# Kernel optimization log

Hardware: AMD Instinct MI355X
Metric: run time of the kernel (lower is better)

Reference implementation:

```python
import jax, jax.numpy as jnp
import numpy as np

D_MODEL = 64
D_K = 64
D_V = 64
N_HEADS = 4
D_FF = 64
D_HALF = 32  # d_model / 2 in the sca_* MLPs


def _layer_norm(x, eps=1e-5):
    m = jnp.mean(x, axis=-1, keepdims=True)
    v = jnp.var(x, axis=-1, keepdims=True)
    return (x - m) / jnp.sqrt(v + eps)


def _sca(u, w1, w2):
    # nn.Sequential(Linear(64,32), ReLU, Linear(32,1)), no bias
    return jax.nn.relu(u @ w1) @ w2  # [B,1,1]


def setup_inputs() -> dict:
    key = jax.random.key(0)
    ks = jax.random.split(key, 20)
    B, L = 128, 512

    def lin(k, fan_in, fan_out):
        bound = 1.0 / np.sqrt(fan_in)
        return jax.random.uniform(k, (fan_in, fan_out), jnp.float32, -bound, bound)

    inp = {
        "input": jax.random.normal(ks[0], (B, L, D_MODEL), jnp.float32),
        "attn_mask": jax.random.bernoulli(ks[1], 0.1, (B, L, L)),
        "input_u": jax.random.normal(ks[2], (B, 1, D_MODEL), jnp.float32),
        "W_Q": lin(ks[3], D_MODEL, N_HEADS * D_K),
        "W_K": lin(ks[4], D_MODEL, N_HEADS * D_K),
        "W_V": lin(ks[5], D_MODEL, N_HEADS * D_V),
        "U_Q": lin(ks[6], D_MODEL, D_K),
        "U_K": lin(ks[7], D_MODEL, D_K),
        "U_V": lin(ks[8], D_MODEL, D_V),
        "sq1": lin(ks[9], D_MODEL, D_HALF),
        "sq2": lin(ks[10], D_HALF, 1),
        "sk1": lin(ks[11], D_MODEL, D_HALF),
        "sk2": lin(ks[12], D_HALF, 1),
        "sv1": lin(ks[13], D_MODEL, D_HALF),
        "sv2": lin(ks[14], D_HALF, 1),
        "fc": lin(ks[15], N_HEADS * D_V, D_MODEL),
        "ff1": lin(ks[16], D_MODEL, D_FF),
        "ff2": lin(ks[17], D_FF, D_MODEL),
    }
    return inp


def reference(input, attn_mask, input_u, W_Q, W_K, W_V, U_Q, U_K, U_V,
              sq1, sq2, sk1, sk2, sv1, sv2, fc, ff1, ff2):
    B, L, _ = input.shape
    scale = 1.0 / np.sqrt(D_K).astype(np.float32)

    # multi-head projections: [B, H, L, d]
    Q = (input @ W_Q).reshape(B, L, N_HEADS, D_K).transpose(0, 2, 1, 3)
    K = (input @ W_K).reshape(B, L, N_HEADS, D_K).transpose(0, 2, 1, 3)
    V = (input @ W_V).reshape(B, L, N_HEADS, D_V).transpose(0, 2, 1, 3)

    # per-batch scalar gates from input_u: [B,1,1]
    s_q = _sca(input_u, sq1, sq2)
    s_k = _sca(input_u, sk1, sk2)
    s_v = _sca(input_u, sv1, sv2)

    # single-head u projections, gated; broadcast over heads later
    u_Q = (input @ U_Q) * s_q  # [B, L, d_k]
    u_K = (input @ U_K) * s_k  # [B, L, d_k]
    u_V = (input @ U_V) * s_v  # [B, L, d_v]

    scores = jnp.einsum('bhqd,bhkd->bhqk', Q, K) * scale
    scores = scores + (jnp.einsum('bqd,bkd->bqk', u_Q, u_K) * scale)[:, None]
    scores = jnp.where(attn_mask[:, None], jnp.float32(-1e9), scores)
    attn = jax.nn.softmax(scores, axis=-1)  # [B, H, L, L]

    context = jnp.einsum('bhqk,bhkd->bhqd', attn, V + u_V[:, None])
    context = context.transpose(0, 2, 1, 3).reshape(B, L, N_HEADS * D_V)

    out = context @ fc  # dropout is identity in eval
    enc = _layer_norm(out + input)

    # position-wise FFN with residual + layernorm
    ffn = jax.nn.relu(enc @ ff1) @ ff2
    enc_outputs = _layer_norm(ffn + enc)
    return (enc_outputs, attn)
```

## Files before the change

### kernel.cpp

```cpp
#include <hip/hip_runtime.h>

typedef unsigned char  u8;
typedef unsigned short u16;
typedef unsigned int   u32;

typedef __attribute__((ext_vector_type(8))) short bf16x8;
typedef __attribute__((ext_vector_type(4))) float f32x4;

__device__ __forceinline__ u16 f2bf(float f) {
  union { float f; u32 u; } v; v.f = f;
  u32 u = v.u;
  u32 r = u + 0x7fffu + ((u >> 16) & 1u);
  return (u16)(r >> 16);
}
__device__ __forceinline__ float bf2f(u16 h) {
  union { u32 u; float f; } v; v.u = ((u32)h) << 16;
  return v.f;
}
__device__ __forceinline__ bf16x8 pack8(float4 a, float4 b) {
  bf16x8 r;
  r[0] = (short)f2bf(a.x); r[1] = (short)f2bf(a.y);
  r[2] = (short)f2bf(a.z); r[3] = (short)f2bf(a.w);
  r[4] = (short)f2bf(b.x); r[5] = (short)f2bf(b.y);
  r[6] = (short)f2bf(b.z); r[7] = (short)f2bf(b.w);
  return r;
}
__device__ __forceinline__ f32x4 mfma16(bf16x8 a, bf16x8 b, f32x4 c) {
  return __builtin_amdgcn_mfma_f32_16x16x32_bf16(a, b, c, 0, 0, 0);
}

__global__ void kflaginit(u32* flags) { flags[0] = 0; flags[1] = 0; }

__global__ void kscan(const u32* __restrict__ m, u32* __restrict__ flags) {
  int gid = blockIdx.x * 256 + threadIdx.x;
  const uint4* p = (const uint4*)m;
  u32 gt = 0, fp = 0;
#pragma unroll
  for (int i = 0; i < 4; ++i) {
    uint4 v = p[gid * 4 + i];
    gt |= (u32)((v.x > 1u) | (v.y > 1u) | (v.z > 1u) | (v.w > 1u));
    fp |= (u32)((v.x == 0x3F800000u) | (v.y == 0x3F800000u) |
                (v.z == 0x3F800000u) | (v.w == 0x3F800000u));
  }
  if (gt) flags[0] = 1;
  if (fp) flags[1] = 1;
}

__global__ void kconv(const void* __restrict__ m, const u32* __restrict__ flags,
                      u8* __restrict__ out) {
  int gid = blockIdx.x * 256 + threadIdx.x;
  u32 isf = flags[1], isb = flags[0];
  uchar4 o;
  if (isf) {
    float4 v = ((const float4*)m)[gid];
    o.x = v.x != 0.f; o.y = v.y != 0.f; o.z = v.z != 0.f; o.w = v.w != 0.f;
  } else if (isb) {
    uchar4 v = ((const uchar4*)m)[gid];
    o.x = v.x != 0; o.y = v.y != 0; o.z = v.z != 0; o.w = v.w != 0;
  } else {
    uint4 v = ((const uint4*)m)[gid];
    o.x = v.x != 0; o.y = v.y != 0; o.z = v.z != 0; o.w = v.w != 0;
  }
  ((uchar4*)out)[gid] = o;
}

__global__ void kgates(const float* __restrict__ iu,
                       const float* __restrict__ q1, const float* __restrict__ q2,
                       const float* __restrict__ k1, const float* __restrict__ k2,
                       const float* __restrict__ v1, const float* __restrict__ v2,
                       float* __restrict__ gates) {
  int b = blockIdx.x, t = threadIdx.x;
  __shared__ float u[64];
  u[t] = iu[b * 64 + t];
  __syncthreads();
  const float* w1[3] = {q1, k1, v1};
  const float* w2[3] = {q2, k2, v2};
#pragma unroll
  for (int m = 0; m < 3; ++m) {
    float p = 0.f;
    if (t < 32) {
      float h = 0.f;
      for (int i = 0; i < 64; ++i) h += u[i] * w1[m][i * 32 + t];
      h = fmaxf(h, 0.f);
      p = h * w2[m][t];
    }
    for (int off = 32; off >= 1; off >>= 1) p += __shfl_xor(p, off);
    if (t == 0) gates[m * 128 + b] = p;
  }
}

__launch_bounds__(256, 1)
__global__ void kproj_qk(const float* __restrict__ x,
                         const float* __restrict__ wq, const float* __restrict__ uq,
                         const float* __restrict__ wk, const float* __restrict__ uk,
                         const float* __restrict__ gates,
                         u16* __restrict__ qc, u16* __restrict__ qu,
                         u16* __restrict__ kc, u16* __restrict__ ku) {
  __shared__ u16 XT[64 * 136];
  __shared__ u16 WT[640 * 72];
  int b = blockIdx.x >> 3, l0 = (blockIdx.x & 7) * 64, t = threadIdx.x;
  {
    int tok = t >> 2, i0 = (t & 3) * 16;
    const float4* s = (const float4*)(x + ((size_t)(b * 512 + l0 + tok)) * 64 + i0);
    *(bf16x8*)&XT[tok * 136 + i0]     = pack8(s[0], s[1]);
    *(bf16x8*)&XT[tok * 136 + i0 + 8] = pack8(s[2], s[3]);
  }
  for (int i = 0; i < 64; ++i) { int e = t + i * 256; WT[(e & 255) * 72 + (e >> 8)] = (short)f2bf(wq[e]); }
  for (int i = 0; i < 16; ++i) { int e = t + i * 256; WT[(256 + (e & 63)) * 72 + (e >> 6)] = (short)f2bf(uq[e]); }
  for (int i = 0; i < 64; ++i) { int e = t + i * 256; WT[(320 + (e & 255)) * 72 + (e >> 8)] = (short)f2bf(wk[e]); }
  for (int i = 0; i < 16; ++i) { int e = t + i * 256; WT[(576 + (e & 63)) * 72 + (e >> 6)] = (short)f2bf(uk[e]); }
  __syncthreads();

  int w = t >> 6, lane = t & 63, lrow = lane & 15, lgrp = lane >> 4;
  bf16x8 af[4][2];
#pragma unroll
  for (int m = 0; m < 4; ++m)
#pragma unroll
    for (int fs = 0; fs < 2; ++fs)
      af[m][fs] = *(const bf16x8*)&XT[(m * 16 + lrow) * 136 + fs * 32 + lgrp * 8];

  float sq = gates[b], sk = gates[128 + b];
  const f32x4 fz = {0.f, 0.f, 0.f, 0.f};
#pragma unroll
  for (int part = 0; part < 2; ++part) {
    f32x4 acc[4][5];
#pragma unroll
    for (int m = 0; m < 4; ++m)
#pragma unroll
      for (int nt = 0; nt < 5; ++nt) acc[m][nt] = fz;
#pragma unroll
    for (int fs = 0; fs < 2; ++fs)
#pragma unroll
      for (int nt = 0; nt < 5; ++nt) {
        bf16x8 bf = *(const bf16x8*)&WT[(part * 320 + w * 80 + nt * 16 + lrow) * 72 + fs * 32 + lgrp * 8];
#pragma unroll
        for (int m = 0; m < 4; ++m)
          acc[m][nt] = mfma16(af[m][fs], bf, acc[m][nt]);
      }
    u16* dstC = part ? kc : qc;
    u16* dstU = part ? ku : qu;
    float presc = part ? 1.0f : 0.125f;
    float g = (part ? sk : sq) * presc;
#pragma unroll
    for (int nt = 0; nt < 5; ++nt) {
      int ncol = w * 80 + nt * 16 + lrow;
#pragma unroll
      for (int m = 0; m < 4; ++m)
#pragma unroll
        for (int j = 0; j < 4; ++j) {
          int l = l0 + m * 16 + lgrp * 4 + j;
          float v = acc[m][nt][j];
          if (ncol < 256) {
            dstC[(((size_t)(b * 4 + (ncol >> 6)) * 512) + l) * 64 + (ncol & 63)] = (short)f2bf(v * presc);
          } else {
            dstU[((size_t)b * 512 + l) * 64 + (ncol - 256)] = (short)f2bf(v * g);
          }
        }
    }
  }
}

__launch_bounds__(256, 1)
__global__ void kproj_v(const float* __restrict__ x,
                        const float* __restrict__ wv, const float* __restrict__ uv,
                        const float* __restrict__ gates, u16* __restrict__ vpt) {
  __shared__ u16 XT[64 * 136];
  __shared__ u16 WT[320 * 72];
  __shared__ float Vs[64 * 328];
  int b = blockIdx.x >> 3, l0 = (blockIdx.x & 7) * 64, t = threadIdx.x;
  {
    int tok = t >> 2, i0 = (t & 3) * 16;
    const float4* s = (const float4*)(x + ((size_t)(b * 512 + l0 + tok)) * 64 + i0);
    *(bf16x8*)&XT[tok * 136 + i0]     = pack8(s[0], s[1]);
    *(bf16x8*)&XT[tok * 136 + i0 + 8] = pack8(s[2], s[3]);
  }
  for (int i = 0; i < 64; ++i) { int e = t + i * 256; WT[(e & 255) * 72 + (e >> 8)] = (short)f2bf(wv[e]); }
  for (int i = 0; i < 16; ++i) { int e = t + i * 256; WT[(256 + (e & 63)) * 72 + (e >> 6)] = (short)f2bf(uv[e]); }
  __syncthreads();

  int w = t >> 6, lane = t & 63, lrow = lane & 15, lgrp = lane >> 4;
  bf16x8 af[4][2];
#pragma unroll
  for (int m = 0; m < 4; ++m)
#pragma unroll
    for (int fs = 0; fs < 2; ++fs)
      af[m][fs] = *(const bf16x8*)&XT[(m * 16 + lrow) * 136 + fs * 32 + lgrp * 8];

  const f32x4 fz = {0.f, 0.f, 0.f, 0.f};
  f32x4 acc[4][5];
#pragma unroll
  for (int m = 0; m < 4; ++m)
#pragma unroll
    for (int nt = 0; nt < 5; ++nt) acc[m][nt] = fz;
#pragma unroll
  for (int fs = 0; fs < 2; ++fs)
#pragma unroll
    for (int nt = 0; nt < 5; ++nt) {
      bf16x8 bf = *(const bf16x8*)&WT[(w * 80 + nt * 16 + lrow) * 72 + fs * 32 + lgrp * 8];
#pragma unroll
      for (int m = 0; m < 4; ++m)
        acc[m][nt] = mfma16(af[m][fs], bf, acc[m][nt]);
    }
#pragma unroll
  for (int nt = 0; nt < 5; ++nt)
#pragma unroll
    for (int m = 0; m < 4; ++m)
#pragma unroll
      for (int j = 0; j < 4; ++j)
        Vs[(m * 16 + lgrp * 4 + j) * 328 + w * 80 + nt * 16 + lrow] = acc[m][nt][j];
  __syncthreads();

  float sv = gates[256 + b];
#pragma unroll
  for (int p = 0; p < 4; ++p) {
    int hd = p * 64 + (t >> 2);
    int d = hd & 63;
    int tok0 = (t & 3) * 16;
    bf16x8 v0, v1;
#pragma unroll
    for (int i = 0; i < 8; ++i) {
      int tok = tok0 + i;
      v0[i] = (short)f2bf(Vs[tok * 328 + hd] + Vs[tok * 328 + 256 + d] * sv);
    }
#pragma unroll
    for (int i = 0; i < 8; ++i) {
      int tok = tok0 + 8 + i;
      v1[i] = (short)f2bf(Vs[tok * 328 + hd] + Vs[tok * 328 + 256 + d] * sv);
    }
    size_t base = (((size_t)(b * 4 + (hd >> 6)) * 64) + d) * 512 + l0 + tok0;
    *(bf16x8*)&vpt[base] = v0;
    *(bf16x8*)&vpt[base + 8] = v1;
  }
}

__launch_bounds__(256, 1)
__global__ void kattn(const u16* __restrict__ qc, const u16* __restrict__ qu,
                      const u16* __restrict__ kc, const u16* __restrict__ ku,
                      const u16* __restrict__ vpt, const u8* __restrict__ maskb,
                      float* __restrict__ aout, u16* __restrict__ ctx) {
  __shared__ char smem[133120];
  u16* QT = (u16*)smem;
  u16* KT = (u16*)(smem + 17408);
  u16* Pl = (u16*)smem;
  u16* Vt = (u16*)(smem + 66560);

  int bid = blockIdx.x;
  int bh = bid >> 3, qt = bid & 7;
  int b = bh >> 2, hh = bh & 3;
  int q0 = qt * 64;
  int t = threadIdx.x, w = t >> 6, lane = t & 63, lrow = lane & 15, lgrp = lane >> 4;

  {
    int tok = t >> 2, c0 = (t & 3) * 32;
    const u16* src = (c0 < 64)
      ? qc + ((size_t)bh * 512 + q0 + tok) * 64 + c0
      : qu + ((size_t)b  * 512 + q0 + tok) * 64 + (c0 - 64);
#pragma unroll
    for (int i = 0; i < 4; ++i)
      *(bf16x8*)&QT[tok * 136 + c0 + i * 8] = *(const bf16x8*)&src[i * 8];
  }
  {
    int d = t >> 2, c0 = (t & 3) * 128;
    const u16* src = vpt + ((size_t)bh * 64 + d) * 512 + c0;
#pragma unroll
    for (int i = 0; i < 16; ++i)
      *(bf16x8*)&Vt[d * 520 + c0 + i * 8] = *(const bf16x8*)&src[i * 8];
  }

  const f32x4 fz = {0.f, 0.f, 0.f, 0.f};
  f32x4 sacc[32];
#pragma unroll
  for (int i = 0; i < 32; ++i) sacc[i] = fz;

#pragma unroll
  for (int kt = 0; kt < 4; ++kt) {
    __syncthreads();
    {
      int r = t >> 1, c0 = (t & 1) * 64;
      const u16* src = (c0 == 0)
        ? kc + ((size_t)bh * 512 + kt * 128 + r) * 64
        : ku + ((size_t)b  * 512 + kt * 128 + r) * 64;
#pragma unroll
      for (int i = 0; i < 8; ++i)
        *(bf16x8*)&KT[r * 136 + c0 + i * 8] = *(const bf16x8*)&src[i * 8];
    }
    __syncthreads();
#pragma unroll
    for (int fs = 0; fs < 4; ++fs) {
      bf16x8 a = *(const bf16x8*)&QT[(w * 16 + lrow) * 136 + fs * 32 + lgrp * 8];
#pragma unroll
      for (int nt = 0; nt < 8; ++nt) {
        bf16x8 bf = *(const bf16x8*)&KT[(nt * 16 + lrow) * 136 + fs * 32 + lgrp * 8];
        sacc[kt * 8 + nt] = mfma16(a, bf, sacc[kt * 8 + nt]);
      }
    }
  }
  __syncthreads();

  int qloc0 = w * 16 + lgrp * 4;
  const u8* mrow = maskb + ((size_t)b * 512 + q0 + qloc0) * 512;
  float mj[4] = {-3.0e38f, -3.0e38f, -3.0e38f, -3.0e38f};
#pragma unroll
  for (int i = 0; i < 32; ++i) {
    int kpos = (i >> 3) * 128 + (i & 7) * 16 + lrow;
#pragma unroll
    for (int j = 0; j < 4; ++j) {
      float s = sacc[i][j];
      if (mrow[(size_t)j * 512 + kpos]) s = -1.0e9f;
      sacc[i][j] = s;
      mj[j] = fmaxf(mj[j], s);
    }
  }
#pragma unroll
  for (int j = 0; j < 4; ++j) {
    mj[j] = fmaxf(mj[j], __shfl_xor(mj[j], 1));
    mj[j] = fmaxf(mj[j], __shfl_xor(mj[j], 2));
    mj[j] = fmaxf(mj[j], __shfl_xor(mj[j], 4));
    mj[j] = fmaxf(mj[j], __shfl_xor(mj[j], 8));
  }
  float lj[4] = {0.f, 0.f, 0.f, 0.f};
#pragma unroll
  for (int i = 0; i < 32; ++i)
#pragma unroll
    for (int j = 0; j < 4; ++j) {
      float p = __expf(sacc[i][j] - mj[j]);
      sacc[i][j] = p;
      lj[j] += p;
    }
#pragma unroll
  for (int j = 0; j < 4; ++j) {
    lj[j] += __shfl_xor(lj[j], 1);
    lj[j] += __shfl_xor(lj[j], 2);
    lj[j] += __shfl_xor(lj[j], 4);
    lj[j] += __shfl_xor(lj[j], 8);
  }
  float inv[4];
#pragma unroll
  for (int j = 0; j < 4; ++j) inv[j] = 1.0f / lj[j];

  size_t ab = ((size_t)bh * 512 + q0 + qloc0) * 512;
#pragma unroll
  for (int i = 0; i < 32; ++i) {
    int kpos = (i >> 3) * 128 + (i & 7) * 16 + lrow;
#pragma unroll
    for (int j = 0; j < 4; ++j) {
      float aval = sacc[i][j] * inv[j];
      aout[ab + (size_t)j * 512 + kpos] = aval;
      Pl[(qloc0 + j) * 520 + kpos] = (short)f2bf(aval);
    }
  }

  f32x4 cacc[4];
#pragma unroll
  for (int nt = 0; nt < 4; ++nt) cacc[nt] = fz;
#pragma unroll
  for (int ks = 0; ks < 16; ++ks) {
    bf16x8 a = *(const bf16x8*)&Pl[(w * 16 + lrow) * 520 + ks * 32 + lgrp * 8];
#pragma unroll
    for (int nt = 0; nt < 4; ++nt) {
      bf16x8 bf = *(const bf16x8*)&Vt[(nt * 16 + lrow) * 520 + ks * 32 + lgrp * 8];
      cacc[nt] = mfma16(a, bf, cacc[nt]);
    }
  }
#pragma unroll
  for (int nt = 0; nt < 4; ++nt)
#pragma unroll
    for (int j = 0; j < 4; ++j) {
      int q = q0 + qloc0 + j;
      ctx[((size_t)b * 512 + q) * 256 + hh * 64 + nt * 16 + lrow] = (short)f2bf(cacc[nt][j]);
    }
}

__launch_bounds__(256, 1)
__global__ void kffn(const u16* __restrict__ ctx, const float* __restrict__ x,
                     const float* __restrict__ fcw, const float* __restrict__ f1w,
                     const float* __restrict__ f2w, float* __restrict__ out) {
  __shared__ u16 CT[64 * 264];
  __shared__ u16 FCT[64 * 264];
  __shared__ u16 F1T[64 * 72];
  __shared__ u16 F2T[64 * 72];
  __shared__ float ENC[64 * 68];
  __shared__ u16 EBF[64 * 72];
  __shared__ u16 HBF[64 * 72];
  int b = blockIdx.x >> 3, l0 = (blockIdx.x & 7) * 64, t = threadIdx.x;
  {
    int tok = t >> 2, c0 = (t & 3) * 64;
    const u16* src = ctx + ((size_t)(b * 512 + l0 + tok)) * 256 + c0;
#pragma unroll
    for (int i = 0; i < 8; ++i)
      *(bf16x8*)&CT[tok * 264 + c0 + i * 8] = *(const bf16x8*)&src[i * 8];
  }
  for (int i = 0; i < 64; ++i) { int e = t + i * 256; FCT[(e & 63) * 264 + (e >> 6)] = (short)f2bf(fcw[e]); }
  for (int i = 0; i < 16; ++i) { int e = t + i * 256; F1T[(e & 63) * 72 + (e >> 6)] = (short)f2bf(f1w[e]); }
  for (int i = 0; i < 16; ++i) { int e = t + i * 256; F2T[(e & 63) * 72 + (e >> 6)] = (short)f2bf(f2w[e]); }
  __syncthreads();

  int w = t >> 6, lane = t & 63, lrow = lane & 15, lgrp = lane >> 4;
  int row = w * 16 + lgrp * 4;
  const f32x4 fz = {0.f, 0.f, 0.f, 0.f};

  f32x4 acc[4];
#pragma unroll
  for (int nt = 0; nt < 4; ++nt) acc[nt] = fz;
#pragma unroll
  for (int ks = 0; ks < 8; ++ks) {
    bf16x8 a = *(const bf16x8*)&CT[(w * 16 + lrow) * 264 + ks * 32 + lgrp * 8];
#pragma unroll
    for (int nt = 0; nt < 4; ++nt)
      acc[nt] = mfma16(a, *(const bf16x8*)&FCT[(nt * 16 + lrow) * 264 + ks * 32 + lgrp * 8], acc[nt]);
  }
  const float* xb = x + ((size_t)(b * 512 + l0)) * 64;
#pragma unroll
  for (int nt = 0; nt < 4; ++nt)
#pragma unroll
    for (int j = 0; j < 4; ++j)
      acc[nt][j] += xb[(row + j) * 64 + nt * 16 + lrow];

  float mean[4], rstd[4];
#pragma unroll
  for (int j = 0; j < 4; ++j) {
    float s = acc[0][j] + acc[1][j] + acc[2][j] + acc[3][j];
    s += __shfl_xor(s, 1); s += __shfl_xor(s, 2); s += __shfl_xor(s, 4); s += __shfl_xor(s, 8);
    mean[j] = s * 0.015625f;
  }
#pragma unroll
  for (int j = 0; j < 4; ++j) {
    float d0 = acc[0][j] - mean[j], d1 = acc[1][j] - mean[j];
    float d2 = acc[2][j] - mean[j], d3 = acc[3][j] - mean[j];
    float s = d0 * d0 + d1 * d1 + d2 * d2 + d3 * d3;
    s += __shfl_xor(s, 1); s += __shfl_xor(s, 2); s += __shfl_xor(s, 4); s += __shfl_xor(s, 8);
    rstd[j] = 1.0f / sqrtf(s * 0.015625f + 1e-5f);
  }
#pragma unroll
  for (int nt = 0; nt < 4; ++nt)
#pragma unroll
    for (int j = 0; j < 4; ++j) {
      float v = (acc[nt][j] - mean[j]) * rstd[j];
      ENC[(row + j) * 68 + nt * 16 + lrow] = v;
      EBF[(row + j) * 72 + nt * 16 + lrow] = (short)f2bf(v);
    }

  f32x4 h4[4];
#pragma unroll
  for (int nt = 0; nt < 4; ++nt) h4[nt] = fz;
#pragma unroll
  for (int ks = 0; ks < 2; ++ks) {
    bf16x8 a = *(const bf16x8*)&EBF[(w * 16 + lrow) * 72 + ks * 32 + lgrp * 8];
#pragma unroll
    for (int nt = 0; nt < 4; ++nt)
      h4[nt] = mfma16(a, *(const bf16x8*)&F1T[(nt * 16 + lrow) * 72 + ks * 32 + lgrp * 8], h4[nt]);
  }
#pragma unroll
  for (int nt = 0; nt < 4; ++nt)
#pragma unroll
    for (int j = 0; j < 4; ++j)
      HBF[(row + j) * 72 + nt * 16 + lrow] = (short)f2bf(fmaxf(h4[nt][j], 0.f));

  f32x4 o4[4];
#pragma unroll
  for (int nt = 0; nt < 4; ++nt) o4[nt] = fz;
#pragma unroll
  for (int ks = 0; ks < 2; ++ks) {
    bf16x8 a = *(const bf16x8*)&HBF[(w * 16 + lrow) * 72 + ks * 32 + lgrp * 8];
#pragma unroll
    for (int nt = 0; nt < 4; ++nt)
      o4[nt] = mfma16(a, *(const bf16x8*)&F2T[(nt * 16 + lrow) * 72 + ks * 32 + lgrp * 8], o4[nt]);
  }
#pragma unroll
  for (int nt = 0; nt < 4; ++nt)
#pragma unroll
    for (int j = 0; j < 4; ++j)
      o4[nt][j] += ENC[(row + j) * 68 + nt * 16 + lrow];

  float mean2[4], rstd2[4];
#pragma unroll
  for (int j = 0; j < 4; ++j) {
    float s = o4[0][j] + o4[1][j] + o4[2][j] + o4[3][j];
    s += __shfl_xor(s, 1); s += __shfl_xor(s, 2); s += __shfl_xor(s, 4); s += __shfl_xor(s, 8);
    mean2[j] = s * 0.015625f;
  }
#pragma unroll
  for (int j = 0; j < 4; ++j) {
    float d0 = o4[0][j] - mean2[j], d1 = o4[1][j] - mean2[j];
    float d2 = o4[2][j] - mean2[j], d3 = o4[3][j] - mean2[j];
    float s = d0 * d0 + d1 * d1 + d2 * d2 + d3 * d3;
    s += __shfl_xor(s, 1); s += __shfl_xor(s, 2); s += __shfl_xor(s, 4); s += __shfl_xor(s, 8);
    rstd2[j] = 1.0f / sqrtf(s * 0.015625f + 1e-5f);
  }
#pragma unroll
  for (int nt = 0; nt < 4; ++nt)
#pragma unroll
    for (int j = 0; j < 4; ++j)
      out[((size_t)(b * 512 + l0) + row + j) * 64 + nt * 16 + lrow] =
          (o4[nt][j] - mean2[j]) * rstd2[j];
}

extern "C" void kernel_launch(void* const* d_in, const int* in_sizes, int n_in,
                              void* d_out, int out_size, void* d_ws, size_t ws_size,
                              hipStream_t stream) {
  const float* x   = (const float*)d_in[0];
  const void*  msk = d_in[1];
  const float* iu  = (const float*)d_in[2];
  const float* wq  = (const float*)d_in[3];
  const float* wk  = (const float*)d_in[4];
  const float* wv  = (const float*)d_in[5];
  const float* uq  = (const float*)d_in[6];
  const float* uk  = (const float*)d_in[7];
  const float* uv  = (const float*)d_in[8];
  const float* q1  = (const float*)d_in[9];
  const float* q2  = (const float*)d_in[10];
  const float* k1  = (const float*)d_in[11];
  const float* k2  = (const float*)d_in[12];
  const float* v1  = (const float*)d_in[13];
  const float* v2  = (const float*)d_in[14];
  const float* fcw = (const float*)d_in[15];
  const float* f1w = (const float*)d_in[16];
  const float* f2w = (const float*)d_in[17];
  float* out = (float*)d_out;

  char* ws = (char*)d_ws;
  u32*   flags = (u32*)ws;
  float* gates = (float*)(ws + 64);
  u16* qc  = (u16*)(ws + 4096);
  u16* qu  = (u16*)(ws + 33558528);
  u16* kc  = (u16*)(ws + 41947136);
  u16* ku  = (u16*)(ws + 75501568);
  u16* vpt = (u16*)(ws + 83890176);
  u8*  mb  = (u8*) (ws + 117444608);
  u16* ctx = (u16*)(ws + 150999040);

  kflaginit<<<dim3(1), dim3(1), 0, stream>>>(flags);
  kscan<<<dim3(1024), dim3(256), 0, stream>>>((const u32*)msk, flags);
  kconv<<<dim3(32768), dim3(256), 0, stream>>>(msk, flags, mb);
  kgates<<<dim3(128), dim3(64), 0, stream>>>(iu, q1, q2, k1, k2, v1, v2, gates);
  kproj_qk<<<dim3(1024), dim3(256), 0, stream>>>(x, wq, uq, wk, uk, gates, qc, qu, kc, ku);
  kproj_v<<<dim3(1024), dim3(256), 0, stream>>>(x, wv, uv, gates, vpt);
  kattn<<<dim3(4096), dim3(256), 0, stream>>>(qc, qu, kc, ku, vpt, mb, out + 4194304, ctx);
  kffn<<<dim3(1024), dim3(256), 0, stream>>>(ctx, x, fcw, f1w, f2w, out);
}
```

Baseline: 538.1 us.

## Split attention key range across two wave groups and shrink LDS for occupancy

The attention kernel now runs 512 threads, with two wave groups each handling half the keys for the same 64 queries. Row max and row sum are combined through shared memory, and V plus the probability tile are streamed in 128-key chunks instead of being held whole. This cuts LDS from about 130KB to 52KB and halves the per-thread accumulator registers, so more blocks can be resident per CU. Blocks are also remapped so consecutive block IDs touch different batches and heads, which changes how mask and K reuse falls across the machine. The cost is extra barriers and cross-wave reductions.

```diff
diff --git a/kernel.cpp b/kernel.cpp
--- a/kernel.cpp
+++ b/kernel.cpp
@@ -233,81 +233,79 @@
   }
 }
 
-__launch_bounds__(256, 1)
+__launch_bounds__(512, 4)
 __global__ void kattn(const u16* __restrict__ qc, const u16* __restrict__ qu,
                       const u16* __restrict__ kc, const u16* __restrict__ ku,
                       const u16* __restrict__ vpt, const u8* __restrict__ maskb,
                       float* __restrict__ aout, u16* __restrict__ ctx) {
-  __shared__ char smem[133120];
+  __shared__ char smem[53248];
   u16* QT = (u16*)smem;
   u16* KT = (u16*)(smem + 17408);
-  u16* Pl = (u16*)smem;
-  u16* Vt = (u16*)(smem + 66560);
+  float* SMm = (float*)(smem + 52224);
+  float* SMl = (float*)(smem + 52736);
+  u16* Vt = (u16*)smem;
+  u16* Pl = (u16*)(smem + 17408);
 
   int bid = blockIdx.x;
-  int bh = bid >> 3, qt = bid & 7;
-  int b = bh >> 2, hh = bh & 3;
+  int logical = (bid & 7) * 512 + (bid >> 3);
+  int b = logical >> 5;
+  int r5 = logical & 31;
+  int qt = r5 >> 2, hh = r5 & 3;
+  int bh = b * 4 + hh;
   int q0 = qt * 64;
+
   int t = threadIdx.x, w = t >> 6, lane = t & 63, lrow = lane & 15, lgrp = lane >> 4;
+  int qsub = w & 3, g = w >> 2, g64 = g * 64;
 
   {
-    int tok = t >> 2, c0 = (t & 3) * 32;
+    int tok = t >> 3, c0 = (t & 7) * 16;
     const u16* src = (c0 < 64)
       ? qc + ((size_t)bh * 512 + q0 + tok) * 64 + c0
       : qu + ((size_t)b  * 512 + q0 + tok) * 64 + (c0 - 64);
-#pragma unroll
-    for (int i = 0; i < 4; ++i)
-      *(bf16x8*)&QT[tok * 136 + c0 + i * 8] = *(const bf16x8*)&src[i * 8];
-  }
-  {
-    int d = t >> 2, c0 = (t & 3) * 128;
-    const u16* src = vpt + ((size_t)bh * 64 + d) * 512 + c0;
-#pragma unroll
-    for (int i = 0; i < 16; ++i)
-      *(bf16x8*)&Vt[d * 520 + c0 + i * 8] = *(const bf16x8*)&src[i * 8];
+    *(bf16x8*)&QT[tok * 136 + c0]     = *(const bf16x8*)&src[0];
+    *(bf16x8*)&QT[tok * 136 + c0 + 8] = *(const bf16x8*)&src[8];
   }
 
   const f32x4 fz = {0.f, 0.f, 0.f, 0.f};
-  f32x4 sacc[32];
-#pragma unroll
-  for (int i = 0; i < 32; ++i) sacc[i] = fz;
+  f32x4 acc[16];
+#pragma unroll
+  for (int i = 0; i < 16; ++i) acc[i] = fz;
 
 #pragma unroll
   for (int kt = 0; kt < 4; ++kt) {
     __syncthreads();
     {
-      int r = t >> 1, c0 = (t & 1) * 64;
-      const u16* src = (c0 == 0)
-        ? kc + ((size_t)bh * 512 + kt * 128 + r) * 64
-        : ku + ((size_t)b  * 512 + kt * 128 + r) * 64;
-#pragma unroll
-      for (int i = 0; i < 8; ++i)
+      int r = t >> 2, c0 = (t & 3) * 32;
+      const u16* src = (c0 < 64)
+        ? kc + ((size_t)bh * 512 + kt * 128 + r) * 64 + c0
+        : ku + ((size_t)b  * 512 + kt * 128 + r) * 64 + (c0 - 64);
+#pragma unroll
+      for (int i = 0; i < 4; ++i)
         *(bf16x8*)&KT[r * 136 + c0 + i * 8] = *(const bf16x8*)&src[i * 8];
     }
     __syncthreads();
 #pragma unroll
     for (int fs = 0; fs < 4; ++fs) {
-      bf16x8 a = *(const bf16x8*)&QT[(w * 16 + lrow) * 136 + fs * 32 + lgrp * 8];
-#pragma unroll
-      for (int nt = 0; nt < 8; ++nt) {
-        bf16x8 bf = *(const bf16x8*)&KT[(nt * 16 + lrow) * 136 + fs * 32 + lgrp * 8];
-        sacc[kt * 8 + nt] = mfma16(a, bf, sacc[kt * 8 + nt]);
+      bf16x8 a = *(const bf16x8*)&QT[(qsub * 16 + lrow) * 136 + fs * 32 + lgrp * 8];
+#pragma unroll
+      for (int nt = 0; nt < 4; ++nt) {
+        bf16x8 bf = *(const bf16x8*)&KT[(g64 + nt * 16 + lrow) * 136 + fs * 32 + lgrp * 8];
+        acc[kt * 4 + nt] = mfma16(a, bf, acc[kt * 4 + nt]);
       }
     }
   }
-  __syncthreads();
-
-  int qloc0 = w * 16 + lgrp * 4;
+
+  int qloc0 = qsub * 16 + lgrp * 4;
   const u8* mrow = maskb + ((size_t)b * 512 + q0 + qloc0) * 512;
   float mj[4] = {-3.0e38f, -3.0e38f, -3.0e38f, -3.0e38f};
 #pragma unroll
-  for (int i = 0; i < 32; ++i) {
-    int kpos = (i >> 3) * 128 + (i & 7) * 16 + lrow;
+  for (int i = 0; i < 16; ++i) {
+    int kpos = (i >> 2) * 128 + g64 + (i & 3) * 16 + lrow;
 #pragma unroll
     for (int j = 0; j < 4; ++j) {
-      float s = sacc[i][j];
+      float s = acc[i][j];
       if (mrow[(size_t)j * 512 + kpos]) s = -1.0e9f;
-      sacc[i][j] = s;
+      acc[i][j] = s;
       mj[j] = fmaxf(mj[j], s);
     }
   }
@@ -318,13 +316,21 @@
     mj[j] = fmaxf(mj[j], __shfl_xor(mj[j], 4));
     mj[j] = fmaxf(mj[j], __shfl_xor(mj[j], 8));
   }
+  if (lrow == 0) {
+#pragma unroll
+    for (int j = 0; j < 4; ++j) SMm[g64 + qloc0 + j] = mj[j];
+  }
+  __syncthreads();
+  float gm[4];
+#pragma unroll
+  for (int j = 0; j < 4; ++j) gm[j] = fmaxf(SMm[qloc0 + j], SMm[64 + qloc0 + j]);
   float lj[4] = {0.f, 0.f, 0.f, 0.f};
 #pragma unroll
-  for (int i = 0; i < 32; ++i)
+  for (int i = 0; i < 16; ++i)
 #pragma unroll
     for (int j = 0; j < 4; ++j) {
-      float p = __expf(sacc[i][j] - mj[j]);
-      sacc[i][j] = p;
+      float p = __expf(acc[i][j] - gm[j]);
+      acc[i][j] = p;
       lj[j] += p;
     }
 #pragma unroll
@@ -334,41 +340,59 @@
     lj[j] += __shfl_xor(lj[j], 4);
     lj[j] += __shfl_xor(lj[j], 8);
   }
+  if (lrow == 0) {
+#pragma unroll
+    for (int j = 0; j < 4; ++j) SMl[g64 + qloc0 + j] = lj[j];
+  }
+  __syncthreads();
   float inv[4];
 #pragma unroll
-  for (int j = 0; j < 4; ++j) inv[j] = 1.0f / lj[j];
+  for (int j = 0; j < 4; ++j) inv[j] = 1.0f / (SMl[qloc0 + j] + SMl[64 + qloc0 + j]);
 
   size_t ab = ((size_t)bh * 512 + q0 + qloc0) * 512;
 #pragma unroll
-  for (int i = 0; i < 32; ++i) {
-    int kpos = (i >> 3) * 128 + (i & 7) * 16 + lrow;
+  for (int i = 0; i < 16; ++i) {
+    int kpos = (i >> 2) * 128 + g64 + (i & 3) * 16 + lrow;
 #pragma unroll
     for (int j = 0; j < 4; ++j) {
-      float aval = sacc[i][j] * inv[j];
-      aout[ab + (size_t)j * 512 + kpos] = aval;
-      Pl[(qloc0 + j) * 520 + kpos] = (short)f2bf(aval);
-    }
-  }
-
-  f32x4 cacc[4];
-#pragma unroll
-  for (int nt = 0; nt < 4; ++nt) cacc[nt] = fz;
-#pragma unroll
-  for (int ks = 0; ks < 16; ++ks) {
-    bf16x8 a = *(const bf16x8*)&Pl[(w * 16 + lrow) * 520 + ks * 32 + lgrp * 8];
-#pragma unroll
-    for (int nt = 0; nt < 4; ++nt) {
-      bf16x8 bf = *(const bf16x8*)&Vt[(nt * 16 + lrow) * 520 + ks * 32 + lgrp * 8];
-      cacc[nt] = mfma16(a, bf, cacc[nt]);
-    }
-  }
-#pragma unroll
-  for (int nt = 0; nt < 4; ++nt)
-#pragma unroll
-    for (int j = 0; j < 4; ++j) {
-      int q = q0 + qloc0 + j;
-      ctx[((size_t)b * 512 + q) * 256 + hh * 64 + nt * 16 + lrow] = (short)f2bf(cacc[nt][j]);
-    }
+      float av = acc[i][j] * inv[j];
+      acc[i][j] = av;
+      aout[ab + (size_t)j * 512 + kpos] = av;
+    }
+  }
+
+  f32x4 cacc[2] = {fz, fz};
+#pragma unroll
+  for (int c = 0; c < 4; ++c) {
+    {
+      int d = t >> 3, c0 = (t & 7) * 16;
+      const u16* src = vpt + ((size_t)bh * 64 + d) * 512 + c * 128 + c0;
+      *(bf16x8*)&Vt[d * 136 + c0]     = *(const bf16x8*)&src[0];
+      *(bf16x8*)&Vt[d * 136 + c0 + 8] = *(const bf16x8*)&src[8];
+    }
+#pragma unroll
+    for (int nt = 0; nt < 4; ++nt)
+#pragma unroll
+      for (int j = 0; j < 4; ++j)
+        Pl[(qloc0 + j) * 136 + g64 + nt * 16 + lrow] = (short)f2bf(acc[c * 4 + nt][j]);
+    __syncthreads();
+#pragma unroll
+    for (int ks = 0; ks < 4; ++ks) {
+      bf16x8 a = *(const bf16x8*)&Pl[(qsub * 16 + lrow) * 136 + ks * 32 + lgrp * 8];
+#pragma unroll
+      for (int nt2 = 0; nt2 < 2; ++nt2) {
+        bf16x8 bf = *(const bf16x8*)&Vt[(g * 32 + nt2 * 16 + lrow) * 136 + ks * 32 + lgrp * 8];
+        cacc[nt2] = mfma16(a, bf, cacc[nt2]);
+      }
+    }
+    __syncthreads();
+  }
+#pragma unroll
+  for (int nt2 = 0; nt2 < 2; ++nt2)
+#pragma unroll
+    for (int j = 0; j < 4; ++j)
+      ctx[((size_t)b * 512 + q0 + qloc0 + j) * 256 + hh * 64 + g * 32 + nt2 * 16 + lrow] =
+          (short)f2bf(cacc[nt2][j]);
 }
 
 __launch_bounds__(256, 1)
@@ -535,6 +559,6 @@
   kgates<<<dim3(128), dim3(64), 0, stream>>>(iu, q1, q2, k1, k2, v1, v2, gates);
   kproj_qk<<<dim3(1024), dim3(256), 0, stream>>>(x, wq, uq, wk, uk, gates, qc, qu, kc, ku);
   kproj_v<<<dim3(1024), dim3(256), 0, stream>>>(x, wv, uv, gates, vpt);
-  kattn<<<dim3(4096), dim3(256), 0, stream>>>(qc, qu, kc, ku, vpt, mb, out + 4194304, ctx);
+  kattn<<<dim3(4096), dim3(512), 0, stream>>>(qc, qu, kc, ku, vpt, mb, out + 4194304, ctx);
   kffn<<<dim3(1024), dim3(256), 0, stream>>>(ctx, x, fcw, f1w, f2w, out);
 }
```

After: 463.7 us. 1.16x faster.
